# Kernel tuning notes

Hardware: AMD Instinct MI355X
Metric: run time of the kernel (lower is better)

## Reference

```python
import jax, jax.numpy as jnp
import numpy as np

B, T, E, H = 4, 2048, 1024, 16
HD = E // H

def setup_inputs() -> dict:
    key = jax.random.key(0)
    ks = jax.random.split(key, 5)
    s = 1.0 / np.sqrt(E)
    return {
        "x": jax.random.normal(ks[0], (B, T, E), dtype=jnp.float32),
        "mask": jnp.zeros((B, T), dtype=bool),
        "qkv_w": jax.random.uniform(ks[1], (3 * E, E), jnp.float32, -s, s),
        "qkv_b": jax.random.uniform(ks[2], (3 * E,), jnp.float32, -s, s),
        "proj_w": jax.random.uniform(ks[3], (E, E), jnp.float32, -s, s),
        "proj_b": jax.random.uniform(ks[4], (E,), jnp.float32, -s, s),
    }

def reference(x, mask, qkv_w, qkv_b, proj_w, proj_b):
    b, t, e = x.shape
    qkv = x @ qkv_w.T + qkv_b                      # [b,t,3e]
    q, k, v = jnp.split(qkv, 3, axis=2)
    # [b,t,e] -> [b,h,t,hd]
    q = q.reshape(b, t, H, HD).transpose(0, 2, 1, 3)
    k = k.reshape(b, t, H, HD).transpose(0, 2, 1, 3)
    v = v.reshape(b, t, H, HD).transpose(0, 2, 1, 3)
    scale = 1.0 / np.sqrt(HD)
    attn = jnp.einsum('bhqd,bhkd->bhqk', q, k) * scale
    # mask: True -> -inf, broadcast over heads and query positions
    neg = jnp.where(mask, -jnp.inf, 0.0).astype(attn.dtype)  # [b,t]
    attn = attn + neg[:, None, None, :]
    attn = jax.nn.softmax(attn, axis=-1)
    # dropout layers in eval mode (deterministic reference)
    out = jnp.einsum('bhqk,bhkd->bhqd', attn, v)   # [b,h,t,hd]
    out = out.transpose(0, 2, 1, 3).reshape(b, t, e)
    return out @ proj_w.T + proj_b
```

## Files before the change

### kernel.cpp

```cpp
#include <hip/hip_runtime.h>
#include <stdint.h>

#define Bz  4
#define Tz  2048
#define Ez  1024
#define Hz  16
#define HDz 64
#define Mz  (Bz*Tz)

typedef short bf16x8 __attribute__((ext_vector_type(8)));
typedef float f32x4  __attribute__((ext_vector_type(4)));
typedef unsigned short u16;

__device__ __forceinline__ u16 f2bf(float f) {
  return (u16)((__builtin_bit_cast(uint32_t, f) + 0x8000u) >> 16);
}
__device__ __forceinline__ uint32_t pack2bf(float a, float b) {
  uint32_t ua = __builtin_bit_cast(uint32_t, a) + 0x8000u;
  uint32_t ub = __builtin_bit_cast(uint32_t, b) + 0x8000u;
  return __builtin_amdgcn_perm(ub, ua, 0x07060302u);
}

#if __has_builtin(__builtin_amdgcn_exp2f)
#define EXP2(x) __builtin_amdgcn_exp2f(x)
#else
#define EXP2(x) exp2f(x)
#endif

__device__ __forceinline__ void gl2lds16(const u16* g, u16* l) {
  __builtin_amdgcn_global_load_lds((const __attribute__((address_space(1))) void*)g,
                                   (__attribute__((address_space(3))) void*)l, 16, 0, 0);
}

__global__ void cvt_f32_bf16_3(const float* __restrict__ s0, u16* __restrict__ d0, int n0,
                               const float* __restrict__ s1, u16* __restrict__ d1, int n1,
                               const float* __restrict__ s2, u16* __restrict__ d2, int n2) {
  int j = blockIdx.x * blockDim.x + threadIdx.x;
  const float* s; u16* d;
  if (j < n0) { s = s0; d = d0; }
  else {
    j -= n0;
    if (j < n1) { s = s1; d = d1; }
    else { j -= n1; if (j >= n2) return; s = s2; d = d2; }
  }
  float4 f = ((const float4*)s)[j];
  uint2 o;
  o.x = pack2bf(f.x, f.y);
  o.y = pack2bf(f.z, f.w);
  ((uint2*)d)[j] = o;
}

template<int MODE>
__global__ __launch_bounds__(256, 2) void gemm_bt(
    const u16* __restrict__ A, const u16* __restrict__ Bw,
    const float* __restrict__ bias,
    u16* __restrict__ qo, u16* __restrict__ ko, u16* __restrict__ vto,
    float* __restrict__ fo)
{
  __shared__ u16 Ab[2][128*64];
  __shared__ u16 Bb[2][128*64];
  const int tid  = threadIdx.x;
  const int lane = tid & 63;
  const int wid  = tid >> 6;
  const int quad = lane >> 4;
  const int cl   = lane & 15;
  const int wm   = wid >> 1, wn = wid & 1;
  const int bm   = blockIdx.y * 128;
  const int bn   = blockIdx.x * 128;
  const int srow = lane >> 3;
  const int ssw  = lane & 7;

  f32x4 acc[4][4] = {};

  auto stage = [&](int kt, int buf) {
#pragma unroll
    for (int s = 0; s < 4; ++s) {
      const int r  = wid*32 + s*8 + srow;
      const int cc = ssw ^ (r & 7);
      gl2lds16(A + (size_t)(bm + r)*Ez + kt + cc*8, &Ab[buf][(wid*32 + s*8)*64]);
    }
#pragma unroll
    for (int s = 0; s < 4; ++s) {
      const int r  = wid*32 + s*8 + srow;
      const int cc = ssw ^ (r & 7);
      gl2lds16(Bw + (size_t)(bn + r)*Ez + kt + cc*8, &Bb[buf][(wid*32 + s*8)*64]);
    }
  };

  stage(0, 0);

#pragma unroll 2
  for (int it = 0; it < 16; ++it) {
    const int bufc = it & 1;
    __syncthreads();
    if (it < 15) stage((it+1)*64, bufc^1);
    const u16* AB = &Ab[bufc][0];
    const u16* BB = &Bb[bufc][0];
#pragma unroll
    for (int ks = 0; ks < 2; ++ks) {
      bf16x8 af[4], bfr[4];
#pragma unroll
      for (int mi = 0; mi < 4; ++mi) {
        const int row = wm*64 + mi*16 + cl;
        const int ch  = (ks*4 + quad) ^ (row & 7);
        af[mi] = *(const bf16x8*)&AB[row*64 + ch*8];
      }
#pragma unroll
      for (int ni = 0; ni < 4; ++ni) {
        const int row = wn*64 + ni*16 + cl;
        const int ch  = (ks*4 + quad) ^ (row & 7);
        bfr[ni] = *(const bf16x8*)&BB[row*64 + ch*8];
      }
#pragma unroll
      for (int mi = 0; mi < 4; ++mi)
#pragma unroll
        for (int ni = 0; ni < 4; ++ni)
          acc[mi][ni] = __builtin_amdgcn_mfma_f32_16x16x32_bf16(af[mi], bfr[ni], acc[mi][ni], 0, 0, 0);
    }
  }

  const float qsc = 0.125f * 1.4426950408889634f;
#pragma unroll
  for (int ni = 0; ni < 4; ++ni) {
    const int n   = bn + wn*64 + ni*16 + cl;
    const float bv = bias[n];
#pragma unroll
    for (int mi = 0; mi < 4; ++mi) {
      const int m0 = bm + wm*64 + mi*16 + quad*4;
      if (MODE == 0) {
        const int which = n >> 10;
        const int e = n & 1023;
        const int h = e >> 6, d = e & 63;
        const int b = m0 >> 11, t0 = m0 & 2047;
        if (which == 2) {
          uint2 pk;
          pk.x = pack2bf(acc[mi][ni][0] + bv, acc[mi][ni][1] + bv);
          pk.y = pack2bf(acc[mi][ni][2] + bv, acc[mi][ni][3] + bv);
          *(uint2*)&vto[(((size_t)(b*Hz + h))*HDz + d)*Tz + t0] = pk;
        } else {
#pragma unroll
          for (int r = 0; r < 4; ++r) {
            const int t = t0 + r;
            float val = acc[mi][ni][r] + bv;
            if (which == 0) qo[(((size_t)(b*Hz + h))*Tz + t)*HDz + d] = f2bf(val * qsc);
            else            ko[(((size_t)(b*Hz + h))*Tz + t)*HDz + d] = f2bf(val);
          }
        }
      } else {
#pragma unroll
        for (int r = 0; r < 4; ++r)
          fo[(size_t)(m0 + r)*Ez + n] = acc[mi][ni][r] + bv;
      }
    }
  }
}

__global__ __launch_bounds__(256, 4) void attn_flash(
    const u16* __restrict__ Q, const u16* __restrict__ K,
    const u16* __restrict__ Vt, const unsigned char* __restrict__ mask,
    u16* __restrict__ ctx)
{
  __shared__ u16 Kb[2][32*64];
  __shared__ u16 Vb[2][64*32];
  __shared__ u16 Pb[4*2*16*36];

  const int tid  = threadIdx.x;
  const int lane = tid & 63;
  const int wid  = tid >> 6;
  const int quad = lane >> 4;
  const int cl   = lane & 15;
  const int bh   = blockIdx.x;
  const int b    = bh >> 4;
  const int qrw  = blockIdx.y * 128 + wid * 32;
  u16* Pw = &Pb[wid * (2*16*36)];

  const int krow = wid*8  + (lane >> 3);
  const int kch  = (lane & 7) ^ (krow & 7);
  const int vrow = wid*16 + (lane >> 2);
  const int vch  = (lane & 3) ^ ((vrow >> 1) & 3);
  const u16* Kg = K  + ((size_t)bh*Tz + krow)*HDz + kch*8;
  const u16* Vg = Vt + ((size_t)bh*HDz + vrow)*Tz + vch*8;
  u16* KbL[2] = { &Kb[0][(wid*8)*64],  &Kb[1][(wid*8)*64]  };
  u16* VbL[2] = { &Vb[0][(wid*16)*32], &Vb[1][(wid*16)*32] };

  const unsigned char* mrow_p = mask + (size_t)b * Tz;
  bool domask;
  {
    const uint4* mp = (const uint4*)mrow_p;
    uint4 a = mp[lane*2], c = mp[lane*2 + 1];
    uint32_t any = a.x | a.y | a.z | a.w | c.x | c.y | c.z | c.w;
    domask = __any(any != 0);
  }

  bf16x8 aq[2][2];
#pragma unroll
  for (int qb = 0; qb < 2; ++qb) {
    const u16* Qg = Q + ((size_t)bh*Tz + qrw + qb*16 + cl)*HDz;
    aq[qb][0] = *(const bf16x8*)(Qg + quad*8);
    aq[qb][1] = *(const bf16x8*)(Qg + 32 + quad*8);
  }

  bf16x8 ones;
#pragma unroll
  for (int i = 0; i < 8; ++i) ones[i] = (short)0x3F80;

  f32x4 o[2][4] = {};
  f32x4 lacc[2] = {};

  gl2lds16(Kg, KbL[0]);
  gl2lds16(Vg, VbL[0]);

#pragma unroll 2
  for (int it = 0; it < 64; ++it) {
    const int bufc = it & 1;
    __syncthreads();
    if (it < 63) {
      gl2lds16(Kg + (size_t)(it+1)*32*HDz, KbL[bufc^1]);
      gl2lds16(Vg + (it+1)*32,             VbL[bufc^1]);
    }
    const u16* KB = &Kb[bufc][0];
    const u16* VB = &Vb[bufc][0];
    const int kt = it * 32;

    f32x4 st[2][2] = {};
#pragma unroll
    for (int kb = 0; kb < 2; ++kb) {
      bf16x8 kf[2];
#pragma unroll
      for (int nb = 0; nb < 2; ++nb) {
        const int row = nb*16 + cl;
        const int ch  = (kb*4 + quad) ^ (row & 7);
        kf[nb] = *(const bf16x8*)&KB[row*64 + ch*8];
      }
#pragma unroll
      for (int qb = 0; qb < 2; ++qb)
#pragma unroll
        for (int nb = 0; nb < 2; ++nb)
          st[qb][nb] = __builtin_amdgcn_mfma_f32_16x16x32_bf16(kf[nb], aq[qb][kb], st[qb][nb], 0, 0, 0);
    }

    if (domask) {
#pragma unroll
      for (int nb = 0; nb < 2; ++nb) {
        uint32_t mm = *(const uint32_t*)&mrow_p[kt + nb*16 + quad*4];
        if (mm) {
#pragma unroll
          for (int qb = 0; qb < 2; ++qb) {
            if (mm & 0x000000ffu) st[qb][nb][0] = -INFINITY;
            if (mm & 0x0000ff00u) st[qb][nb][1] = -INFINITY;
            if (mm & 0x00ff0000u) st[qb][nb][2] = -INFINITY;
            if (mm & 0xff000000u) st[qb][nb][3] = -INFINITY;
          }
        }
      }
    }

#pragma unroll
    for (int qb = 0; qb < 2; ++qb) {
      u16* Pq = Pw + qb * (16*36);
#pragma unroll
      for (int nb = 0; nb < 2; ++nb) {
        uint2 pk;
        pk.x = pack2bf(EXP2(st[qb][nb][0]), EXP2(st[qb][nb][1]));
        pk.y = pack2bf(EXP2(st[qb][nb][2]), EXP2(st[qb][nb][3]));
        *(uint2*)&Pq[cl*36 + (nb*4 + quad)*4] = pk;
      }
    }

    bf16x8 pf[2];
#pragma unroll
    for (int qb = 0; qb < 2; ++qb) {
      const u16* pr = &Pw[qb*(16*36) + cl*36 + quad*8];
      uint2 lo = *(const uint2*)pr;
      uint2 hi = *(const uint2*)(pr + 4);
      int4 pi = { (int)lo.x, (int)lo.y, (int)hi.x, (int)hi.y };
      pf[qb] = __builtin_bit_cast(bf16x8, pi);
      lacc[qb] = __builtin_amdgcn_mfma_f32_16x16x32_bf16(pf[qb], ones, lacc[qb], 0, 0, 0);
    }
#pragma unroll
    for (int db = 0; db < 4; ++db) {
      const int row = db*16 + cl;
      const int ch  = quad ^ ((row >> 1) & 3);
      bf16x8 bv = *(const bf16x8*)&VB[row*32 + ch*8];
#pragma unroll
      for (int qb = 0; qb < 2; ++qb)
        o[qb][db] = __builtin_amdgcn_mfma_f32_16x16x32_bf16(pf[qb], bv, o[qb][db], 0, 0, 0);
    }
  }

#pragma unroll
  for (int qb = 0; qb < 2; ++qb) {
#pragma unroll
    for (int r = 0; r < 4; ++r) {
      const float inv = 1.0f / lacc[qb][r];
      const int t = qrw + qb*16 + quad*4 + r;
      const size_t base = ((size_t)b*Tz + t)*Ez + (size_t)(bh & 15)*HDz;
#pragma unroll
      for (int db = 0; db < 4; ++db) {
        ctx[base + db*16 + cl] = f2bf(o[qb][db][r] * inv);
      }
    }
  }
}

extern "C" void kernel_launch(void* const* d_in, const int* in_sizes, int n_in,
                              void* d_out, int out_size, void* d_ws, size_t ws_size,
                              hipStream_t stream) {
  (void)in_sizes; (void)n_in; (void)out_size; (void)ws_size;
  const float* x      = (const float*)d_in[0];
  const unsigned char* mask = (const unsigned char*)d_in[1];
  const float* qkv_w  = (const float*)d_in[2];
  const float* qkv_b  = (const float*)d_in[3];
  const float* proj_w = (const float*)d_in[4];
  const float* proj_b = (const float*)d_in[5];
  float* out = (float*)d_out;

  char* ws = (char*)d_ws;
  u16* xb   = (u16*)(ws + 0);
  u16* wqb  = (u16*)(ws + 16777216);
  u16* wpb  = (u16*)(ws + 23068672);
  u16* Qb   = (u16*)(ws + 25165824);
  u16* Kb_  = (u16*)(ws + 41943040);
  u16* Vtb  = (u16*)(ws + 58720256);
  u16* ctxb = (u16*)(ws + 75497472);

  cvt_f32_bf16_3<<<12288, 256, 0, stream>>>(x, xb, 2097152,
                                            qkv_w, wqb, 786432,
                                            proj_w, wpb, 262144);

  gemm_bt<0><<<dim3(24, 64), 256, 0, stream>>>(xb, wqb, qkv_b, Qb, Kb_, Vtb, nullptr);
  attn_flash<<<dim3(64, 16), 256, 0, stream>>>(Qb, Kb_, Vtb, mask, ctxb);
  gemm_bt<1><<<dim3(8, 64), 256, 0, stream>>>(ctxb, wpb, proj_b, nullptr, nullptr, nullptr, out);
}
```

Baseline: 268.9 us.

## Double KV tile to 64 and replace LDS P round-trip with permlane swaps

The attention kernel now stages 64 keys per iteration instead of 32, which halves the number of loop iterations and barriers and gives each wave more MFMA work per synchronization. The transpose of the P tile into MFMA operand layout no longer goes through a shared-memory write and read. It uses v_permlane32_swap and v_permlane16_swap register exchanges instead, removing the P buffer and its LDS traffic. In exchange, shared memory for K/V doubles and register pressure rises from the larger score tile, which may affect occupancy under the 4-block launch bound.

```diff
diff --git a/kernel.cpp b/kernel.cpp
--- a/kernel.cpp
+++ b/kernel.cpp
@@ -160,9 +160,8 @@
     const u16* __restrict__ Vt, const unsigned char* __restrict__ mask,
     u16* __restrict__ ctx)
 {
-  __shared__ u16 Kb[2][32*64];
-  __shared__ u16 Vb[2][64*32];
-  __shared__ u16 Pb[4*2*16*36];
+  __shared__ u16 Kb[2][64*64];
+  __shared__ u16 Vb[2][64*64];
 
   const int tid  = threadIdx.x;
   const int lane = tid & 63;
@@ -172,16 +171,20 @@
   const int bh   = blockIdx.x;
   const int b    = bh >> 4;
   const int qrw  = blockIdx.y * 128 + wid * 32;
-  u16* Pw = &Pb[wid * (2*16*36)];
-
-  const int krow = wid*8  + (lane >> 3);
-  const int kch  = (lane & 7) ^ (krow & 7);
-  const int vrow = wid*16 + (lane >> 2);
-  const int vch  = (lane & 3) ^ ((vrow >> 1) & 3);
-  const u16* Kg = K  + ((size_t)bh*Tz + krow)*HDz + kch*8;
-  const u16* Vg = Vt + ((size_t)bh*HDz + vrow)*Tz + vch*8;
-  u16* KbL[2] = { &Kb[0][(wid*8)*64],  &Kb[1][(wid*8)*64]  };
-  u16* VbL[2] = { &Vb[0][(wid*16)*32], &Vb[1][(wid*16)*32] };
+
+  const int srow = wid*16 + (lane >> 3);
+  const int sch  = (lane & 7) ^ (srow & 7);
+  const u16* Kg = K  + ((size_t)bh*Tz + srow)*HDz + sch*8;
+  const u16* Vg = Vt + ((size_t)bh*HDz + srow)*Tz + sch*8;
+  u16* KbL[2] = { &Kb[0][(wid*16)*64], &Kb[1][(wid*16)*64] };
+  u16* VbL[2] = { &Vb[0][(wid*16)*64], &Vb[1][(wid*16)*64] };
+
+  auto stage = [&](int kt, int buf) {
+    gl2lds16(Kg + (size_t)kt*HDz,           KbL[buf]);
+    gl2lds16(Kg + (size_t)kt*HDz + 8*HDz,   KbL[buf] + 8*64);
+    gl2lds16(Vg + kt,                       VbL[buf]);
+    gl2lds16(Vg + kt + (size_t)8*Tz,        VbL[buf] + 8*64);
+  };
 
   const unsigned char* mrow_p = mask + (size_t)b * Tz;
   bool domask;
@@ -207,27 +210,23 @@
   f32x4 o[2][4] = {};
   f32x4 lacc[2] = {};
 
-  gl2lds16(Kg, KbL[0]);
-  gl2lds16(Vg, VbL[0]);
+  stage(0, 0);
 
 #pragma unroll 2
-  for (int it = 0; it < 64; ++it) {
+  for (int it = 0; it < 32; ++it) {
     const int bufc = it & 1;
     __syncthreads();
-    if (it < 63) {
-      gl2lds16(Kg + (size_t)(it+1)*32*HDz, KbL[bufc^1]);
-      gl2lds16(Vg + (it+1)*32,             VbL[bufc^1]);
-    }
+    if (it < 31) stage((it+1)*64, bufc^1);
     const u16* KB = &Kb[bufc][0];
     const u16* VB = &Vb[bufc][0];
-    const int kt = it * 32;
-
-    f32x4 st[2][2] = {};
+    const int kt = it * 64;
+
+    f32x4 st[2][4] = {};
 #pragma unroll
     for (int kb = 0; kb < 2; ++kb) {
-      bf16x8 kf[2];
-#pragma unroll
-      for (int nb = 0; nb < 2; ++nb) {
+      bf16x8 kf[4];
+#pragma unroll
+      for (int nb = 0; nb < 4; ++nb) {
         const int row = nb*16 + cl;
         const int ch  = (kb*4 + quad) ^ (row & 7);
         kf[nb] = *(const bf16x8*)&KB[row*64 + ch*8];
@@ -235,13 +234,13 @@
 #pragma unroll
       for (int qb = 0; qb < 2; ++qb)
 #pragma unroll
-        for (int nb = 0; nb < 2; ++nb)
+        for (int nb = 0; nb < 4; ++nb)
           st[qb][nb] = __builtin_amdgcn_mfma_f32_16x16x32_bf16(kf[nb], aq[qb][kb], st[qb][nb], 0, 0, 0);
     }
 
     if (domask) {
 #pragma unroll
-      for (int nb = 0; nb < 2; ++nb) {
+      for (int nb = 0; nb < 4; ++nb) {
         uint32_t mm = *(const uint32_t*)&mrow_p[kt + nb*16 + quad*4];
         if (mm) {
 #pragma unroll
@@ -255,36 +254,37 @@
       }
     }
 
+    bf16x8 pf[2][2];
 #pragma unroll
     for (int qb = 0; qb < 2; ++qb) {
-      u16* Pq = Pw + qb * (16*36);
-#pragma unroll
-      for (int nb = 0; nb < 2; ++nb) {
-        uint2 pk;
-        pk.x = pack2bf(EXP2(st[qb][nb][0]), EXP2(st[qb][nb][1]));
-        pk.y = pack2bf(EXP2(st[qb][nb][2]), EXP2(st[qb][nb][3]));
-        *(uint2*)&Pq[cl*36 + (nb*4 + quad)*4] = pk;
-      }
-    }
-
-    bf16x8 pf[2];
-#pragma unroll
-    for (int qb = 0; qb < 2; ++qb) {
-      const u16* pr = &Pw[qb*(16*36) + cl*36 + quad*8];
-      uint2 lo = *(const uint2*)pr;
-      uint2 hi = *(const uint2*)(pr + 4);
-      int4 pi = { (int)lo.x, (int)lo.y, (int)hi.x, (int)hi.y };
-      pf[qb] = __builtin_bit_cast(bf16x8, pi);
-      lacc[qb] = __builtin_amdgcn_mfma_f32_16x16x32_bf16(pf[qb], ones, lacc[qb], 0, 0, 0);
-    }
+#pragma unroll
+      for (int kv = 0; kv < 2; ++kv) {
+        uint32_t ux = pack2bf(EXP2(st[qb][2*kv  ][0]), EXP2(st[qb][2*kv  ][1]));
+        uint32_t uy = pack2bf(EXP2(st[qb][2*kv  ][2]), EXP2(st[qb][2*kv  ][3]));
+        uint32_t vx = pack2bf(EXP2(st[qb][2*kv+1][0]), EXP2(st[qb][2*kv+1][1]));
+        uint32_t vy = pack2bf(EXP2(st[qb][2*kv+1][2]), EXP2(st[qb][2*kv+1][3]));
+        asm("v_permlane32_swap_b32 %0, %1" : "+v"(ux), "+v"(vx));
+        asm("v_permlane32_swap_b32 %0, %1" : "+v"(uy), "+v"(vy));
+        asm("v_permlane16_swap_b32 %0, %1" : "+v"(ux), "+v"(vx));
+        asm("v_permlane16_swap_b32 %0, %1" : "+v"(uy), "+v"(vy));
+        int4 pi = { (int)ux, (int)uy, (int)vx, (int)vy };
+        pf[qb][kv] = __builtin_bit_cast(bf16x8, pi);
+        lacc[qb] = __builtin_amdgcn_mfma_f32_16x16x32_bf16(pf[qb][kv], ones, lacc[qb], 0, 0, 0);
+      }
+    }
+
 #pragma unroll
     for (int db = 0; db < 4; ++db) {
       const int row = db*16 + cl;
-      const int ch  = quad ^ ((row >> 1) & 3);
-      bf16x8 bv = *(const bf16x8*)&VB[row*32 + ch*8];
-#pragma unroll
-      for (int qb = 0; qb < 2; ++qb)
-        o[qb][db] = __builtin_amdgcn_mfma_f32_16x16x32_bf16(pf[qb], bv, o[qb][db], 0, 0, 0);
+      const int r7  = row & 7;
+#pragma unroll
+      for (int kv = 0; kv < 2; ++kv) {
+        const int ch = (kv*4 + quad) ^ r7;
+        bf16x8 bv = *(const bf16x8*)&VB[row*64 + ch*8];
+#pragma unroll
+        for (int qb = 0; qb < 2; ++qb)
+          o[qb][db] = __builtin_amdgcn_mfma_f32_16x16x32_bf16(pf[qb][kv], bv, o[qb][db], 0, 0, 0);
+      }
     }
   }
 
```

Result: no change. 271.1 us (+0.8%).
